# Optimization experiments

Measured on AMD Instinct MI355X. Metric: run time of the kernel, lower is better.

## Reference

```python
import jax, jax.numpy as jnp
import numpy as np

DIM = 256
HEADS = 4
DEPTH = DIM // HEADS
EXPAND = 4
EPS = 1e-3  # keras BatchNormalization default epsilon


def _bn(x, gamma, beta, mean, var):
    # inference-mode batch norm over last axis
    return gamma * (x - mean) * jax.lax.rsqrt(var + EPS) + beta


def setup_inputs() -> dict:
    key = jax.random.key(0)
    ks = jax.random.split(key, 12)
    B, S, D = 4, 2048, DIM
    H = D * EXPAND
    s = 1.0 / np.sqrt(D)
    inp = {
        "x": jax.random.normal(ks[0], (B, S, D), jnp.float32),
        "bn1_gamma": jnp.ones((D,), jnp.float32),
        "bn1_beta": jnp.zeros((D,), jnp.float32),
        "bn1_mean": jax.random.normal(ks[1], (D,), jnp.float32) * 0.1,
        "bn1_var": jnp.abs(jax.random.normal(ks[2], (D,), jnp.float32)) + 0.5,
        "wq": jax.random.normal(ks[3], (D, D), jnp.float32) * s,
        "bq": jnp.zeros((D,), jnp.float32),
        "wk": jax.random.normal(ks[4], (D, D), jnp.float32) * s,
        "bk": jnp.zeros((D,), jnp.float32),
        "wv": jax.random.normal(ks[5], (D, D), jnp.float32) * s,
        "bv": jnp.zeros((D,), jnp.float32),
        "wo": jax.random.normal(ks[6], (D, D), jnp.float32) * s,
        "bo": jnp.zeros((D,), jnp.float32),
        "bn2_gamma": jnp.ones((D,), jnp.float32),
        "bn2_beta": jnp.zeros((D,), jnp.float32),
        "bn2_mean": jax.random.normal(ks[7], (D,), jnp.float32) * 0.1,
        "bn2_var": jnp.abs(jax.random.normal(ks[8], (D,), jnp.float32)) + 0.5,
        "w1": jax.random.normal(ks[9], (D, H), jnp.float32) * s,
        "w2": jax.random.normal(ks[10], (H, D), jnp.float32) * (1.0 / np.sqrt(H)),
    }
    return inp


def reference(x, bn1_gamma, bn1_beta, bn1_mean, bn1_var,
              wq, bq, wk, bk, wv, bv, wo, bo,
              bn2_gamma, bn2_beta, bn2_mean, bn2_var, w1, w2):
    B, S, D = x.shape
    h = _bn(x, bn1_gamma, bn1_beta, bn1_mean, bn1_var)
    # project and split heads -> [B, H, S, depth]
    def heads(t):
        return t.reshape(B, S, HEADS, DEPTH).transpose(0, 2, 1, 3)
    q = heads(h @ wq + bq)
    k = heads(h @ wk + bk)
    v = heads(h @ wv + bv)
    scores = jnp.einsum("bhqd,bhkd->bhqk", q, k) / jnp.sqrt(jnp.float32(DEPTH))
    attn = jax.nn.softmax(scores, axis=-1)
    ctx = jnp.einsum("bhqk,bhkd->bhqd", attn, v)
    ctx = ctx.transpose(0, 2, 1, 3).reshape(B, S, D)
    attn_out = ctx @ wo + bo
    x1 = attn_out + x  # residual (dropout = identity at inference)
    h2 = _bn(x1, bn2_gamma, bn2_beta, bn2_mean, bn2_var)
    m = jax.nn.gelu(h2 @ w1, approximate=False) @ w2
    return m + x1
```

## Files before the change

### kernel.cpp

```cpp
#include <hip/hip_runtime.h>

typedef unsigned short u16;
typedef unsigned int u32;
typedef short short8 __attribute__((ext_vector_type(8)));
typedef short short4v __attribute__((ext_vector_type(4)));
typedef float f32x4 __attribute__((ext_vector_type(4)));

#define EPS 1e-3f
#define C1F 0.18033688011112042f

#if defined(__HIP_DEVICE_COMPILE__)
#define MFMA16(a, b, c) __builtin_amdgcn_mfma_f32_16x16x16bf16_1k(a, b, c, 0, 0, 0)
#else
#define MFMA16(a, b, c) (c)
#endif

static __device__ __forceinline__ u16 f2bf(float f) {
    u32 u = __float_as_uint(f);
    u += 0x7fffu + ((u >> 16) & 1u);
    return (u16)(u >> 16);
}
static __device__ __forceinline__ float bf2f(u16 v) {
    u32 u = (u32)v << 16;
    return __uint_as_float(u);
}
static __device__ __forceinline__ u32 pack_bf2(float a, float b) {
    u32 ua = __float_as_uint(a) + 0x8000u;
    u32 ub = __float_as_uint(b) + 0x8000u;
    return __builtin_amdgcn_perm(ub, ua, 0x07060302u);
}
static __device__ __forceinline__ void async_cp16(const void* g, void* l) {
    __builtin_amdgcn_global_load_lds(
        (const __attribute__((address_space(1))) unsigned int*)g,
        (__attribute__((address_space(3))) unsigned int*)l, 16, 0, 0);
}

__global__ void prep_kernel(const float* __restrict__ wq, const float* __restrict__ wk,
                            const float* __restrict__ wv, const float* __restrict__ wo,
                            const float* __restrict__ w1, const float* __restrict__ w2,
                            const float* __restrict__ bq, const float* __restrict__ bk,
                            const float* __restrict__ bv,
                            const float* __restrict__ g1, const float* __restrict__ b1,
                            const float* __restrict__ m1, const float* __restrict__ v1,
                            const float* __restrict__ g2, const float* __restrict__ b2,
                            const float* __restrict__ m2, const float* __restrict__ v2,
                            u16* __restrict__ wqkvT, u16* __restrict__ woT,
                            u16* __restrict__ w1T, u16* __restrict__ w2T,
                            float* __restrict__ bqkv,
                            float* __restrict__ bn1sc, float* __restrict__ bn1sh,
                            float* __restrict__ bn2sc, float* __restrict__ bn2sh) {
    int idx = blockIdx.x * 256 + threadIdx.x;
    if (idx < 196608) {
        int n = idx >> 8, k = idx & 255;
        float v;
        if (n < 256)      v = wq[k * 256 + n];
        else if (n < 512) v = wk[k * 256 + (n - 256)] * C1F;
        else              v = wv[k * 256 + (n - 512)];
        wqkvT[idx] = f2bf(v);
    } else if (idx < 262144) {
        int i = idx - 196608; int n = i >> 8, k = i & 255;
        woT[i] = f2bf(wo[k * 256 + n]);
    } else if (idx < 524288) {
        int i = idx - 262144; int n = i >> 8, k = i & 255;
        w1T[i] = f2bf(w1[k * 1024 + n]);
    } else if (idx < 786432) {
        int i = idx - 524288; int n = i >> 10, k = i & 1023;
        w2T[i] = f2bf(w2[k * 256 + n]);
    } else if (idx < 787200) {
        int i = idx - 786432;
        bqkv[i] = (i < 256) ? bq[i] : (i < 512 ? bk[i - 256] * C1F : bv[i - 512]);
    } else if (idx < 787456) {
        int i = idx - 787200;
        float sc = g1[i] * rsqrtf(v1[i] + EPS);
        bn1sc[i] = sc; bn1sh[i] = b1[i] - m1[i] * sc;
    } else if (idx < 787712) {
        int i = idx - 787456;
        float sc = g2[i] * rsqrtf(v2[i] + EPS);
        bn2sc[i] = sc; bn2sh[i] = b2[i] - m2[i] * sc;
    }
}

__global__ void bn1_kernel(const float* __restrict__ x, const float* __restrict__ sc,
                           const float* __restrict__ sh, u16* __restrict__ h) {
    int idx = blockIdx.x * 256 + threadIdx.x;
    int base = idx * 4;
    int c = base & 255;
    float4 xv = *(const float4*)(x + base);
    float4 s4 = *(const float4*)(sc + c);
    float4 h4 = *(const float4*)(sh + c);
    ushort4 pk;
    pk.x = f2bf(fmaf(xv.x, s4.x, h4.x));
    pk.y = f2bf(fmaf(xv.y, s4.y, h4.y));
    pk.z = f2bf(fmaf(xv.z, s4.z, h4.z));
    pk.w = f2bf(fmaf(xv.w, s4.w, h4.w));
    *(ushort4*)(h + base) = pk;
}

template <int EPI>
__global__ __launch_bounds__(256) void gemm64(
        const u16* __restrict__ A, const u16* __restrict__ Bt,
        int M, int N, int K,
        const float* __restrict__ bias, const float* __restrict__ resid,
        float* __restrict__ out_f32, u16* __restrict__ out_bf,
        u16* __restrict__ out_vt,
        const float* __restrict__ b2sc, const float* __restrict__ b2sh) {
    __shared__ u16 abuf[64 * 64];
    __shared__ u16 bbuf[64 * 64];
    const int t = threadIdx.x;
    const int w = t >> 6, lane = t & 63;
    const int l = lane & 15, Q = lane >> 4;
    const int m0 = blockIdx.x * 64;
    const int n0 = blockIdx.y * 64;

    f32x4 acc[4];
#pragma unroll
    for (int nt = 0; nt < 4; ++nt) acc[nt] = (f32x4){0.f, 0.f, 0.f, 0.f};

    for (int k0 = 0; k0 < K; k0 += 64) {
#pragma unroll
        for (int j = 0; j < 2; ++j) {
            int idx = j * 256 + t;
            int r = idx >> 3, c8 = idx & 7;
            int sc = c8 ^ (r & 7);
            async_cp16(A + (size_t)(m0 + r) * K + k0 + sc * 8, abuf + idx * 8);
        }
#pragma unroll
        for (int j = 0; j < 2; ++j) {
            int idx = j * 256 + t;
            int r = idx >> 3, c8 = idx & 7;
            int sc = c8 ^ (r & 7);
            async_cp16(Bt + (size_t)(n0 + r) * K + k0 + sc * 8, bbuf + idx * 8);
        }
        __syncthreads();
#pragma unroll
        for (int kd = 0; kd < 2; ++kd) {
            int ar = w * 16 + l;
            short8 afr = *(const short8*)(abuf + ar * 64 + (((kd * 4 + Q) ^ (ar & 7))) * 8);
#pragma unroll
            for (int nt = 0; nt < 4; ++nt) {
                int r = nt * 16 + l;
                short8 bfr = *(const short8*)(bbuf + r * 64 + (((kd * 4 + Q) ^ (r & 7))) * 8);
                acc[nt] = __builtin_amdgcn_mfma_f32_16x16x32_bf16(afr, bfr, acc[nt], 0, 0, 0);
            }
        }
        __syncthreads();
    }

#pragma unroll
    for (int nt = 0; nt < 4; ++nt) {
        int col = n0 + nt * 16 + l;
        int row0 = m0 + w * 16 + Q * 4;
        if (EPI == 0) {
            float b = bias[col];
            if (col < 512) {
#pragma unroll
                for (int r = 0; r < 4; ++r)
                    out_bf[(size_t)(row0 + r) * 512 + col] = f2bf(acc[nt][r] + b);
            } else {
                ushort4 pk;
                pk.x = f2bf(acc[nt][0] + b);
                pk.y = f2bf(acc[nt][1] + b);
                pk.z = f2bf(acc[nt][2] + b);
                pk.w = f2bf(acc[nt][3] + b);
                *(ushort4*)(out_vt + (size_t)(col - 512) * 8192 + row0) = pk;
            }
        } else {
#pragma unroll
            for (int r = 0; r < 4; ++r) {
                int row = row0 + r;
                float val = acc[nt][r];
                size_t oidx = (size_t)row * N + col;
                if (EPI == 1) {
                    val += bias[col] + resid[oidx];
                    out_f32[oidx] = val;
                    out_bf[oidx] = f2bf(fmaf(val, b2sc[col], b2sh[col]));
                } else if (EPI == 2) {
                    float gl = 0.5f * val * (1.f + erff(val * 0.70710678118654752f));
                    out_bf[oidx] = f2bf(gl);
                } else {
                    out_f32[oidx] = val + resid[oidx];
                }
            }
        }
    }
}

static __device__ __forceinline__ void stage_tiles(const u16* kglob, const u16* vglob,
                                                   u16* kdst, u16* vdst,
                                                   int w, int lane, int kt) {
#pragma unroll
    for (int j = 0; j < 2; ++j) {
        int cw = (w * 2 + j) * 64 + lane;
        int r = cw >> 3;
        int c = (cw & 7) ^ (r & 7);
        async_cp16(kglob + ((size_t)(kt * 64 + r)) * 512 + c * 8, kdst + (w * 2 + j) * 512);
        async_cp16(vglob + ((size_t)r) * 8192 + kt * 64 + c * 8, vdst + (w * 2 + j) * 512);
    }
}

__global__ __launch_bounds__(256) void attn_kernel(const u16* __restrict__ qk,
                                                   const u16* __restrict__ vT,
                                                   u16* __restrict__ opart,
                                                   float* __restrict__ lpart) {
    __shared__ u16 kbuf[4096];
    __shared__ u16 vbuf[4096];
    const int t = threadIdx.x;
    const int w = t >> 6, lane = t & 63;
    const int l = lane & 15, Q = lane >> 4;
    const int qt = blockIdx.x;
    const int bh = blockIdx.y;
    const int sp = blockIdx.z;
    const int bb = bh >> 2, hd = bh & 3;
    const size_t rowbase = (size_t)bb * 2048;
    const int q0 = qt * 128 + w * 32;

    short8 qf[2][2];
#pragma unroll
    for (int qg = 0; qg < 2; ++qg)
#pragma unroll
        for (int kd = 0; kd < 2; ++kd)
            qf[qg][kd] = *(const short8*)(qk + (rowbase + q0 + qg * 16 + l) * 512
                                          + hd * 64 + kd * 32 + Q * 8);

    f32x4 o[2][4];
#pragma unroll
    for (int qg = 0; qg < 2; ++qg)
#pragma unroll
        for (int dt = 0; dt < 4; ++dt) o[qg][dt] = (f32x4){0.f, 0.f, 0.f, 0.f};
    float lacc[2] = {0.f, 0.f};

    const u16* kglob = qk + (rowbase + sp * 256) * 512 + 256 + hd * 64;
    const u16* vglob = vT + ((size_t)(hd * 64)) * 8192 + rowbase + sp * 256;

    for (int kt = 0; kt < 4; ++kt) {
        stage_tiles(kglob, vglob, kbuf, vbuf, w, lane, kt);
        __syncthreads();

        union { u32 u[2]; short4v s4; } pf[2][4];
#pragma unroll
        for (int st = 0; st < 4; ++st) {
            int r = st * 16 + l;
            short8 kf0 = *(const short8*)(kbuf + r * 64 + ((Q) ^ (r & 7)) * 8);
            short8 kf1 = *(const short8*)(kbuf + r * 64 + ((4 + Q) ^ (r & 7)) * 8);
#pragma unroll
            for (int qg = 0; qg < 2; ++qg) {
                f32x4 s = (f32x4){0.f, 0.f, 0.f, 0.f};
                s = __builtin_amdgcn_mfma_f32_16x16x32_bf16(kf0, qf[qg][0], s, 0, 0, 0);
                s = __builtin_amdgcn_mfma_f32_16x16x32_bf16(kf1, qf[qg][1], s, 0, 0, 0);
                float p0 = exp2f(fminf(s[0], 100.f));
                float p1 = exp2f(fminf(s[1], 100.f));
                float p2 = exp2f(fminf(s[2], 100.f));
                float p3 = exp2f(fminf(s[3], 100.f));
                lacc[qg] += (p0 + p1) + (p2 + p3);
                pf[qg][st].u[0] = pack_bf2(p0, p1);
                pf[qg][st].u[1] = pack_bf2(p2, p3);
            }
        }

#pragma unroll
        for (int c = 0; c < 4; ++c) {
#pragma unroll
            for (int dt = 0; dt < 4; ++dt) {
                int r = dt * 16 + l;
                int slot = (2 * c + (Q >> 1)) ^ (r & 7);
                short4v vf = *(const short4v*)(vbuf + r * 64 + slot * 8 + (Q & 1) * 4);
                o[0][dt] = MFMA16(vf, pf[0][c].s4, o[0][dt]);
                o[1][dt] = MFMA16(vf, pf[1][c].s4, o[1][dt]);
            }
        }
        __syncthreads();
    }

#pragma unroll
    for (int qg = 0; qg < 2; ++qg) {
        float v = lacc[qg];
        v += __shfl_xor(v, 16);
        v += __shfl_xor(v, 32);
        lacc[qg] = v;
    }
    u16* ob = opart + (((size_t)sp * 16 + bh) * 2048 + q0) * 64;
#pragma unroll
    for (int qg = 0; qg < 2; ++qg)
#pragma unroll
        for (int dt = 0; dt < 4; ++dt) {
            ushort4 pk;
            pk.x = f2bf(o[qg][dt][0]);
            pk.y = f2bf(o[qg][dt][1]);
            pk.z = f2bf(o[qg][dt][2]);
            pk.w = f2bf(o[qg][dt][3]);
            *(ushort4*)(ob + (size_t)(qg * 16 + l) * 64 + dt * 16 + Q * 4) = pk;
        }
    if (Q == 0) {
        size_t lb = ((size_t)sp * 16 + bh) * 2048 + q0;
        lpart[lb + l] = lacc[0];
        lpart[lb + 16 + l] = lacc[1];
    }
}

__global__ void combine_kernel(const u16* __restrict__ opart,
                               const float* __restrict__ lpart,
                               u16* __restrict__ ctx) {
    int idx = blockIdx.x * 256 + threadIdx.x;
    int e = idx * 4;
    int row = e >> 8, col = e & 255;
    int b = row >> 11, s = row & 2047, h = col >> 6, d = col & 63;
    float a0 = 0.f, a1 = 0.f, a2 = 0.f, a3 = 0.f, lsum = 0.f;
#pragma unroll
    for (int sp = 0; sp < 8; ++sp) {
        size_t pb = (((size_t)sp * 16 + b * 4 + h) * 2048 + s) * 64 + d;
        ushort4 ov = *(const ushort4*)(opart + pb);
        a0 += bf2f(ov.x); a1 += bf2f(ov.y); a2 += bf2f(ov.z); a3 += bf2f(ov.w);
        lsum += lpart[((size_t)sp * 16 + b * 4 + h) * 2048 + s];
    }
    float li = 1.0f / lsum;
    ushort4 pk;
    pk.x = f2bf(a0 * li);
    pk.y = f2bf(a1 * li);
    pk.z = f2bf(a2 * li);
    pk.w = f2bf(a3 * li);
    *(ushort4*)(ctx + e) = pk;
}

extern "C" void kernel_launch(void* const* d_in, const int* in_sizes, int n_in,
                              void* d_out, int out_size, void* d_ws, size_t ws_size,
                              hipStream_t stream) {
    (void)in_sizes; (void)n_in; (void)out_size; (void)ws_size;
    const float* x  = (const float*)d_in[0];
    const float* g1 = (const float*)d_in[1];
    const float* b1 = (const float*)d_in[2];
    const float* m1 = (const float*)d_in[3];
    const float* v1 = (const float*)d_in[4];
    const float* wq = (const float*)d_in[5];
    const float* bq = (const float*)d_in[6];
    const float* wk = (const float*)d_in[7];
    const float* bk = (const float*)d_in[8];
    const float* wv = (const float*)d_in[9];
    const float* bv = (const float*)d_in[10];
    const float* wo = (const float*)d_in[11];
    const float* bo = (const float*)d_in[12];
    const float* g2 = (const float*)d_in[13];
    const float* b2 = (const float*)d_in[14];
    const float* m2 = (const float*)d_in[15];
    const float* v2 = (const float*)d_in[16];
    const float* w1 = (const float*)d_in[17];
    const float* w2 = (const float*)d_in[18];

    char* ws = (char*)d_ws;
    u16*   qkb    = (u16*)(ws + (0ull << 20));
    u16*   vTb    = (u16*)(ws + (8ull << 20));
    u16*   h_buf  = (u16*)(ws + (12ull << 20));
    u16*   ctx    = (u16*)(ws + (16ull << 20));
    float* x1     = (float*)(ws + (20ull << 20));
    u16*   h2     = (u16*)(ws + (28ull << 20));
    u16*   gbuf   = (u16*)(ws + (32ull << 20));
    u16*   opart  = (u16*)(ws + (48ull << 20));
    float* lpart  = (float*)(ws + (80ull << 20));
    u16*   wqkvT  = (u16*)(ws + (81ull << 20));
    u16*   woT    = (u16*)(ws + (82ull << 20));
    u16*   w1T    = (u16*)(ws + (83ull << 20));
    u16*   w2T    = (u16*)(ws + (84ull << 20));
    float* bqkv   = (float*)(ws + (85ull << 20));
    float* bn1sc  = (float*)(ws + (85ull << 20) + 4096);
    float* bn1sh  = (float*)(ws + (85ull << 20) + 8192);
    float* bn2sc  = (float*)(ws + (85ull << 20) + 12288);
    float* bn2sh  = (float*)(ws + (85ull << 20) + 16384);
    float* out    = (float*)d_out;

    prep_kernel<<<3077, 256, 0, stream>>>(wq, wk, wv, wo, w1, w2, bq, bk, bv,
                                          g1, b1, m1, v1, g2, b2, m2, v2,
                                          wqkvT, woT, w1T, w2T, bqkv,
                                          bn1sc, bn1sh, bn2sc, bn2sh);
    bn1_kernel<<<2048, 256, 0, stream>>>(x, bn1sc, bn1sh, h_buf);
    gemm64<0><<<dim3(128, 12), 256, 0, stream>>>(
        h_buf, wqkvT, 8192, 768, 256, bqkv, nullptr, nullptr, qkb, vTb, nullptr, nullptr);
    attn_kernel<<<dim3(16, 16, 8), 256, 0, stream>>>(qkb, vTb, opart, lpart);
    combine_kernel<<<2048, 256, 0, stream>>>(opart, lpart, ctx);
    gemm64<1><<<dim3(128, 4), 256, 0, stream>>>(
        ctx, woT, 8192, 256, 256, bo, x, x1, h2, nullptr, bn2sc, bn2sh);
    gemm64<2><<<dim3(128, 16), 256, 0, stream>>>(
        h2, w1T, 8192, 1024, 256, nullptr, nullptr, nullptr, gbuf, nullptr, nullptr, nullptr);
    gemm64<3><<<dim3(128, 4), 256, 0, stream>>>(
        gbuf, w2T, 8192, 256, 1024, nullptr, x1, out, nullptr, nullptr, nullptr, nullptr);
}
```

Baseline: 193.2 us.

## Double-buffer GEMM and attention tiles, widen attention blocks, coalesce weight prep reads

Adds double-buffered shared memory to the GEMM and attention kernels, so the next K/V or A/B tile is fetched asynchronously while the current one is computed, and drops one barrier per iteration. The attention kernel now uses 512 threads covering 256 queries per block, with half the waves loading K and half loading V, which halves the number of tile loads per query. The weight prep kernel now reads weights contiguously and scatters the transposed writes instead. The cost is twice the shared memory per block, which may lower occupancy. The single barrier per iteration has to be enough to avoid overwriting a buffer that is still being read.

```diff
diff --git a/kernel.cpp b/kernel.cpp
--- a/kernel.cpp
+++ b/kernel.cpp
@@ -51,21 +51,22 @@
                             float* __restrict__ bn2sc, float* __restrict__ bn2sh) {
     int idx = blockIdx.x * 256 + threadIdx.x;
     if (idx < 196608) {
-        int n = idx >> 8, k = idx & 255;
-        float v;
-        if (n < 256)      v = wq[k * 256 + n];
-        else if (n < 512) v = wk[k * 256 + (n - 256)] * C1F;
-        else              v = wv[k * 256 + (n - 512)];
-        wqkvT[idx] = f2bf(v);
+        int sec = idx >> 16;
+        int i = idx & 65535;
+        int k = i >> 8, n = i & 255;
+        const float* w = sec == 0 ? wq : (sec == 1 ? wk : wv);
+        float v = w[i];
+        if (sec == 1) v *= C1F;
+        wqkvT[(sec * 256 + n) * 256 + k] = f2bf(v);
     } else if (idx < 262144) {
-        int i = idx - 196608; int n = i >> 8, k = i & 255;
-        woT[i] = f2bf(wo[k * 256 + n]);
+        int i = idx - 196608; int k = i >> 8, n = i & 255;
+        woT[n * 256 + k] = f2bf(wo[i]);
     } else if (idx < 524288) {
-        int i = idx - 262144; int n = i >> 8, k = i & 255;
-        w1T[i] = f2bf(w1[k * 1024 + n]);
+        int i = idx - 262144; int k = i >> 10, n = i & 1023;
+        w1T[n * 256 + k] = f2bf(w1[i]);
     } else if (idx < 786432) {
-        int i = idx - 524288; int n = i >> 10, k = i & 1023;
-        w2T[i] = f2bf(w2[k * 256 + n]);
+        int i = idx - 524288; int k = i >> 8, n = i & 255;
+        w2T[n * 1024 + k] = f2bf(w2[i]);
     } else if (idx < 787200) {
         int i = idx - 786432;
         bqkv[i] = (i < 256) ? bq[i] : (i < 512 ? bk[i - 256] * C1F : bv[i - 512]);
@@ -104,8 +105,8 @@
         float* __restrict__ out_f32, u16* __restrict__ out_bf,
         u16* __restrict__ out_vt,
         const float* __restrict__ b2sc, const float* __restrict__ b2sh) {
-    __shared__ u16 abuf[64 * 64];
-    __shared__ u16 bbuf[64 * 64];
+    __shared__ u16 abuf[2][4096];
+    __shared__ u16 bbuf[2][4096];
     const int t = threadIdx.x;
     const int w = t >> 6, lane = t & 63;
     const int l = lane & 15, Q = lane >> 4;
@@ -116,34 +117,41 @@
 #pragma unroll
     for (int nt = 0; nt < 4; ++nt) acc[nt] = (f32x4){0.f, 0.f, 0.f, 0.f};
 
-    for (int k0 = 0; k0 < K; k0 += 64) {
+    auto stage = [&](int k0, int b) {
 #pragma unroll
         for (int j = 0; j < 2; ++j) {
             int idx = j * 256 + t;
             int r = idx >> 3, c8 = idx & 7;
             int sc = c8 ^ (r & 7);
-            async_cp16(A + (size_t)(m0 + r) * K + k0 + sc * 8, abuf + idx * 8);
+            async_cp16(A + (size_t)(m0 + r) * K + k0 + sc * 8, abuf[b] + idx * 8);
         }
 #pragma unroll
         for (int j = 0; j < 2; ++j) {
             int idx = j * 256 + t;
             int r = idx >> 3, c8 = idx & 7;
             int sc = c8 ^ (r & 7);
-            async_cp16(Bt + (size_t)(n0 + r) * K + k0 + sc * 8, bbuf + idx * 8);
-        }
+            async_cp16(Bt + (size_t)(n0 + r) * K + k0 + sc * 8, bbuf[b] + idx * 8);
+        }
+    };
+
+    const int nit = K >> 6;
+    stage(0, 0);
+    for (int i = 0; i < nit; ++i) {
         __syncthreads();
+        if (i + 1 < nit) stage((i + 1) << 6, (i + 1) & 1);
+        const u16* ab = abuf[i & 1];
+        const u16* bb = bbuf[i & 1];
 #pragma unroll
         for (int kd = 0; kd < 2; ++kd) {
             int ar = w * 16 + l;
-            short8 afr = *(const short8*)(abuf + ar * 64 + (((kd * 4 + Q) ^ (ar & 7))) * 8);
+            short8 afr = *(const short8*)(ab + ar * 64 + (((kd * 4 + Q) ^ (ar & 7))) * 8);
 #pragma unroll
             for (int nt = 0; nt < 4; ++nt) {
                 int r = nt * 16 + l;
-                short8 bfr = *(const short8*)(bbuf + r * 64 + (((kd * 4 + Q) ^ (r & 7))) * 8);
+                short8 bfr = *(const short8*)(bb + r * 64 + (((kd * 4 + Q) ^ (r & 7))) * 8);
                 acc[nt] = __builtin_amdgcn_mfma_f32_16x16x32_bf16(afr, bfr, acc[nt], 0, 0, 0);
             }
         }
-        __syncthreads();
     }
 
 #pragma unroll
@@ -185,25 +193,28 @@
     }
 }
 
-static __device__ __forceinline__ void stage_tiles(const u16* kglob, const u16* vglob,
-                                                   u16* kdst, u16* vdst,
-                                                   int w, int lane, int kt) {
+static __device__ __forceinline__ void stage_tiles8(const u16* kglob, const u16* vglob,
+                                                    u16* kdst, u16* vdst,
+                                                    int w, int lane, int kt) {
+    const int wp = w & 3;
 #pragma unroll
     for (int j = 0; j < 2; ++j) {
-        int cw = (w * 2 + j) * 64 + lane;
+        int cw = (wp * 2 + j) * 64 + lane;
         int r = cw >> 3;
         int c = (cw & 7) ^ (r & 7);
-        async_cp16(kglob + ((size_t)(kt * 64 + r)) * 512 + c * 8, kdst + (w * 2 + j) * 512);
-        async_cp16(vglob + ((size_t)r) * 8192 + kt * 64 + c * 8, vdst + (w * 2 + j) * 512);
-    }
-}
-
-__global__ __launch_bounds__(256) void attn_kernel(const u16* __restrict__ qk,
+        if (w < 4)
+            async_cp16(kglob + ((size_t)(kt * 64 + r)) * 512 + c * 8, kdst + (wp * 2 + j) * 512);
+        else
+            async_cp16(vglob + ((size_t)r) * 8192 + kt * 64 + c * 8, vdst + (wp * 2 + j) * 512);
+    }
+}
+
+__global__ __launch_bounds__(512) void attn_kernel(const u16* __restrict__ qk,
                                                    const u16* __restrict__ vT,
                                                    u16* __restrict__ opart,
                                                    float* __restrict__ lpart) {
-    __shared__ u16 kbuf[4096];
-    __shared__ u16 vbuf[4096];
+    __shared__ u16 kbuf[2][4096];
+    __shared__ u16 vbuf[2][4096];
     const int t = threadIdx.x;
     const int w = t >> 6, lane = t & 63;
     const int l = lane & 15, Q = lane >> 4;
@@ -212,7 +223,7 @@
     const int sp = blockIdx.z;
     const int bb = bh >> 2, hd = bh & 3;
     const size_t rowbase = (size_t)bb * 2048;
-    const int q0 = qt * 128 + w * 32;
+    const int q0 = qt * 256 + w * 32;
 
     short8 qf[2][2];
 #pragma unroll
@@ -232,16 +243,21 @@
     const u16* kglob = qk + (rowbase + sp * 256) * 512 + 256 + hd * 64;
     const u16* vglob = vT + ((size_t)(hd * 64)) * 8192 + rowbase + sp * 256;
 
+    stage_tiles8(kglob, vglob, kbuf[0], vbuf[0], w, lane, 0);
+
     for (int kt = 0; kt < 4; ++kt) {
-        stage_tiles(kglob, vglob, kbuf, vbuf, w, lane, kt);
         __syncthreads();
+        if (kt < 3)
+            stage_tiles8(kglob, vglob, kbuf[(kt + 1) & 1], vbuf[(kt + 1) & 1], w, lane, kt + 1);
+        const u16* kb = kbuf[kt & 1];
+        const u16* vb = vbuf[kt & 1];
 
         union { u32 u[2]; short4v s4; } pf[2][4];
 #pragma unroll
         for (int st = 0; st < 4; ++st) {
             int r = st * 16 + l;
-            short8 kf0 = *(const short8*)(kbuf + r * 64 + ((Q) ^ (r & 7)) * 8);
-            short8 kf1 = *(const short8*)(kbuf + r * 64 + ((4 + Q) ^ (r & 7)) * 8);
+            short8 kf0 = *(const short8*)(kb + r * 64 + ((Q) ^ (r & 7)) * 8);
+            short8 kf1 = *(const short8*)(kb + r * 64 + ((4 + Q) ^ (r & 7)) * 8);
 #pragma unroll
             for (int qg = 0; qg < 2; ++qg) {
                 f32x4 s = (f32x4){0.f, 0.f, 0.f, 0.f};
@@ -263,12 +279,11 @@
             for (int dt = 0; dt < 4; ++dt) {
                 int r = dt * 16 + l;
                 int slot = (2 * c + (Q >> 1)) ^ (r & 7);
-                short4v vf = *(const short4v*)(vbuf + r * 64 + slot * 8 + (Q & 1) * 4);
+                short4v vf = *(const short4v*)(vb + r * 64 + slot * 8 + (Q & 1) * 4);
                 o[0][dt] = MFMA16(vf, pf[0][c].s4, o[0][dt]);
                 o[1][dt] = MFMA16(vf, pf[1][c].s4, o[1][dt]);
             }
         }
-        __syncthreads();
     }
 
 #pragma unroll
@@ -373,7 +388,7 @@
     bn1_kernel<<<2048, 256, 0, stream>>>(x, bn1sc, bn1sh, h_buf);
     gemm64<0><<<dim3(128, 12), 256, 0, stream>>>(
         h_buf, wqkvT, 8192, 768, 256, bqkv, nullptr, nullptr, qkb, vTb, nullptr, nullptr);
-    attn_kernel<<<dim3(16, 16, 8), 256, 0, stream>>>(qkb, vTb, opart, lpart);
+    attn_kernel<<<dim3(8, 16, 8), 512, 0, stream>>>(qkb, vTb, opart, lpart);
     combine_kernel<<<2048, 256, 0, stream>>>(opart, lpart, ctx);
     gemm64<1><<<dim3(128, 4), 256, 0, stream>>>(
         ctx, woT, 8192, 256, 256, bo, x, x1, h2, nullptr, bn2sc, bn2sh);
```

Result: slower. 199.7 us (+3.4%).
